# Optimization experiments

Measured on AMD Instinct MI355X. Metric: run time of the kernel, lower is better.

The kernel has to match this reference:

```python
import jax, jax.numpy as jnp
import numpy as np

B, T, F, H = 256, 512, 64, 512


def setup_inputs() -> dict:
    key = jax.random.key(0)
    ks = jax.random.split(key, 7)
    s_ih = 1.0 / np.sqrt(H)
    return {
        "x": jax.random.normal(ks[0], (B, T, F), dtype=jnp.float32),
        # PyTorch nn.GRU layout: rows ordered [reset; update; new], each (H, in)
        "W_ih": jax.random.uniform(ks[1], (3 * H, F), minval=-s_ih, maxval=s_ih, dtype=jnp.float32),
        "W_hh": jax.random.uniform(ks[2], (3 * H, H), minval=-s_ih, maxval=s_ih, dtype=jnp.float32),
        "b_ih": jax.random.uniform(ks[3], (3 * H,), minval=-s_ih, maxval=s_ih, dtype=jnp.float32),
        "b_hh": jax.random.uniform(ks[4], (3 * H,), minval=-s_ih, maxval=s_ih, dtype=jnp.float32),
        "head_w": jax.random.uniform(ks[5], (1, H), minval=-s_ih, maxval=s_ih, dtype=jnp.float32),
        "head_b": jax.random.uniform(ks[6], (1,), minval=-s_ih, maxval=s_ih, dtype=jnp.float32),
    }


def _gru_last_hidden(x, W_ih, W_hh, b_ih, b_hh):
    # Precompute input projections for all timesteps: (B, T, 3H)
    gi_all = jnp.einsum("btf,gf->btg", x, W_ih) + b_ih
    gi_all = jnp.swapaxes(gi_all, 0, 1)  # (T, B, 3H) for scan

    def step(h, gi):
        gh = h @ W_hh.T + b_hh  # (B, 3H)
        i_r, i_z, i_n = jnp.split(gi, 3, axis=-1)
        h_r, h_z, h_n = jnp.split(gh, 3, axis=-1)
        r = jax.nn.sigmoid(i_r + h_r)
        z = jax.nn.sigmoid(i_z + h_z)
        n = jnp.tanh(i_n + r * h_n)
        h_new = (1.0 - z) * n + z * h
        return h_new, None

    h0 = jnp.zeros((x.shape[0], W_hh.shape[1]), dtype=x.dtype)
    h_last, _ = jax.lax.scan(step, h0, gi_all)
    return h_last  # (B, H)


def reference(x, W_ih, W_hh, b_ih, b_hh, head_w, head_b):
    last = _gru_last_hidden(x, W_ih, W_hh, b_ih, b_hh)  # out[:, -1, :]
    # head_dropout is identity in eval mode
    y = last @ head_w.T + head_b  # (B, 1)
    return y.squeeze(-1)  # (B,)
```

## Files before the change

### kernel.cpp

```cpp
#include <hip/hip_runtime.h>
#include <hip/hip_bf16.h>

typedef __attribute__((ext_vector_type(4))) float f32x4;
typedef __attribute__((ext_vector_type(8))) short s16x8;
typedef __attribute__((ext_vector_type(4))) unsigned short u16x4;
typedef unsigned long long u64;
typedef unsigned int u32;

#define DEVFN static __device__ __forceinline__

constexpr int B_ = 256, T_ = 512, F_ = 64, H_ = 512;
constexpr int NB = 16;
constexpr int NS = 8;
constexpr int MT = B_ / NB;
constexpr int NT = H_ / NS;
constexpr int NGRID = NB * NS;
constexpr int NTHR = 256;
constexpr int C2 = H_ / 2;

DEVFN unsigned short f2bf(float f) {
  u32 u = __builtin_bit_cast(u32, f);
  u += 0x7fffu + ((u >> 16) & 1u);
  return (unsigned short)(u >> 16);
}

DEVFN float sigmoidf_(float x) { return 1.f / (1.f + __expf(-x)); }
DEVFN float tanhf_(float x) {
  float a = fabsf(x);
  float t = __expf(-2.f * a);
  float r = (1.f - t) / (1.f + t);
  return x < 0.f ? -r : r;
}

__global__ __launch_bounds__(NTHR, 1)
void gru_scan(const float* __restrict__ x, const float* __restrict__ Wih,
              const float* __restrict__ Whh, const float* __restrict__ bih,
              const float* __restrict__ bhh, const float* __restrict__ hw,
              const float* __restrict__ hb, float* __restrict__ out,
              u64* __restrict__ Hpk)
{
  const int tid = threadIdx.x;
  const int lane = tid & 63;
  const int wv = tid >> 6;
  const int gi = (int)blockIdx.x & (NB - 1);
  const int sj = (int)blockIdx.x >> 4;

  __shared__ __align__(16) unsigned char h_lds[2][MT * 1024];
  __shared__ __align__(16) unsigned char x_lds[2][MT * 128];

  const int frow = lane & 15;
  const int g8 = (lane >> 4) * 8;
  const int g16 = (lane >> 4) * 16;
  const int gc = sj * NT + wv * 16 + frow;

  s16x8 whh_f[3][16];
  s16x8 wih_f[3][2];
#pragma unroll
  for (int g = 0; g < 3; ++g) {
    const float* wr = Whh + ((size_t)(g * H_ + gc)) * H_;
#pragma unroll
    for (int kk = 0; kk < 16; ++kk) {
      const float4 p0 = *(const float4*)(wr + kk * 32 + g8);
      const float4 p1 = *(const float4*)(wr + kk * 32 + g8 + 4);
      s16x8 f;
      f[0] = (short)f2bf(p0.x); f[1] = (short)f2bf(p0.y);
      f[2] = (short)f2bf(p0.z); f[3] = (short)f2bf(p0.w);
      f[4] = (short)f2bf(p1.x); f[5] = (short)f2bf(p1.y);
      f[6] = (short)f2bf(p1.z); f[7] = (short)f2bf(p1.w);
      whh_f[g][kk] = f;
    }
    const float* wr2 = Wih + ((size_t)(g * H_ + gc)) * F_;
#pragma unroll
    for (int k2 = 0; k2 < 2; ++k2) {
      const float4 p0 = *(const float4*)(wr2 + k2 * 32 + g8);
      const float4 p1 = *(const float4*)(wr2 + k2 * 32 + g8 + 4);
      s16x8 f;
      f[0] = (short)f2bf(p0.x); f[1] = (short)f2bf(p0.y);
      f[2] = (short)f2bf(p0.z); f[3] = (short)f2bf(p0.w);
      f[4] = (short)f2bf(p1.x); f[5] = (short)f2bf(p1.y);
      f[6] = (short)f2bf(p1.z); f[7] = (short)f2bf(p1.w);
      wih_f[g][k2] = f;
    }
  }

  const float b_r  = bih[gc] + bhh[gc];
  const float b_z  = bih[H_ + gc] + bhh[H_ + gc];
  const float b_in = bih[2 * H_ + gc];
  const float b_hn = bhh[2 * H_ + gc];
  const float hw_l = hw[gc];

  const int aswz = (frow & 7) << 4;
  const int c2own = sj * 32 + wv * 8 + (frow >> 1);

  float hstate[4] = {0.f, 0.f, 0.f, 0.f};

  for (int t = 0; t < T_; ++t) {
    const int p = t & 1;
    if (t > 0) {
      const u64* src = Hpk + ((size_t)p * B_ + gi * MT) * C2 + tid;
      u64 pk[16];
#pragma unroll
      for (int q = 0; q < 16; ++q)
        pk[q] = __hip_atomic_load(src + q * C2, __ATOMIC_RELAXED,
                                  __HIP_MEMORY_SCOPE_AGENT);
      for (;;) {
        bool bad = false;
#pragma unroll
        for (int q = 0; q < 16; ++q) bad |= ((u32)(pk[q] >> 32) != (u32)t);
        if (!__any(bad)) break;
        __builtin_amdgcn_s_sleep(1);
#pragma unroll
        for (int q = 0; q < 16; ++q)
          if ((u32)(pk[q] >> 32) != (u32)t)
            pk[q] = __hip_atomic_load(src + q * C2, __ATOMIC_RELAXED,
                                      __HIP_MEMORY_SCOPE_AGENT);
      }
#pragma unroll
      for (int q = 0; q < 16; ++q)
        *(u32*)(&h_lds[p][q * 1024 + ((tid * 4) ^ ((q & 7) << 4))]) =
            (u32)pk[q];
    }
    {
      const int m = tid >> 4, fs = tid & 15;
      const float4 xv =
          *(const float4*)(x + (((size_t)(gi * MT + m)) * T_ + t) * F_ + fs * 4);
      u16x4 xb;
      xb[0] = f2bf(xv.x); xb[1] = f2bf(xv.y);
      xb[2] = f2bf(xv.z); xb[3] = f2bf(xv.w);
      *(u16x4*)(&x_lds[p][m * 128 + ((fs * 8) ^ ((m & 7) << 4))]) = xb;
    }
    __syncthreads();

    const char* xrow_ptr = (const char*)&x_lds[p][frow * 128];
    const char* hrow_ptr = (const char*)&h_lds[p][frow * 1024];
    f32x4 ar = {0.f, 0.f, 0.f, 0.f}, az = {0.f, 0.f, 0.f, 0.f};
    f32x4 anx = {0.f, 0.f, 0.f, 0.f}, anh = {0.f, 0.f, 0.f, 0.f};
#pragma unroll
    for (int k2 = 0; k2 < 2; ++k2) {
      const s16x8 a = *(const s16x8*)(xrow_ptr + ((k2 * 64 + g16) ^ aswz));
      ar  = __builtin_amdgcn_mfma_f32_16x16x32_bf16(a, wih_f[0][k2], ar, 0, 0, 0);
      az  = __builtin_amdgcn_mfma_f32_16x16x32_bf16(a, wih_f[1][k2], az, 0, 0, 0);
      anx = __builtin_amdgcn_mfma_f32_16x16x32_bf16(a, wih_f[2][k2], anx, 0, 0, 0);
    }
    if (t > 0) {
#pragma unroll
      for (int kk = 0; kk < 16; ++kk) {
        const s16x8 a = *(const s16x8*)(hrow_ptr + ((kk * 64 + g16) ^ aswz));
        ar  = __builtin_amdgcn_mfma_f32_16x16x32_bf16(a, whh_f[0][kk], ar, 0, 0, 0);
        az  = __builtin_amdgcn_mfma_f32_16x16x32_bf16(a, whh_f[1][kk], az, 0, 0, 0);
        anh = __builtin_amdgcn_mfma_f32_16x16x32_bf16(a, whh_f[2][kk], anh, 0, 0, 0);
      }
    }

#pragma unroll
    for (int e = 0; e < 4; ++e) {
      const float rr = sigmoidf_(ar[e] + b_r);
      const float zz = sigmoidf_(az[e] + b_z);
      const float nn = tanhf_(anx[e] + b_in + rr * (anh[e] + b_hn));
      hstate[e] = (1.f - zz) * nn + zz * hstate[e];
    }

    if (t < T_ - 1) {
      unsigned short hbf[4];
#pragma unroll
      for (int e = 0; e < 4; ++e) hbf[e] = f2bf(hstate[e]);
      u64* dstbase = Hpk + ((size_t)((t + 1) & 1) * B_ + gi * MT) * C2;
#pragma unroll
      for (int e = 0; e < 4; ++e) {
        const u32 other = (u32)__shfl_xor((int)hbf[e], 1);
        if (!(lane & 1)) {
          const int m = ((lane >> 4) << 2) + e;
          const u64 val = ((u64)(u32)(t + 1) << 32) |
                          (u64)((u32)hbf[e] | (other << 16));
          __hip_atomic_store(dstbase + m * C2 + c2own, val, __ATOMIC_RELAXED,
                             __HIP_MEMORY_SCOPE_AGENT);
        }
      }
    }
  }

  {
    float part[4];
#pragma unroll
    for (int e = 0; e < 4; ++e) part[e] = hstate[e] * hw_l;
#pragma unroll
    for (int mask = 1; mask < 16; mask <<= 1) {
#pragma unroll
      for (int e = 0; e < 4; ++e) part[e] += __shfl_xor(part[e], mask);
    }
    if ((lane & 15) == 0) {
      const float addb = (sj == 0 && wv == 0) ? hb[0] : 0.f;
#pragma unroll
      for (int e = 0; e < 4; ++e)
        atomicAdd(out + gi * MT + ((lane >> 4) << 2) + e, part[e] + addb);
    }
  }
}

extern "C" void kernel_launch(void* const* d_in, const int* in_sizes, int n_in,
                              void* d_out, int out_size, void* d_ws, size_t ws_size,
                              hipStream_t stream)
{
  const float* x   = (const float*)d_in[0];
  const float* Wih = (const float*)d_in[1];
  const float* Whh = (const float*)d_in[2];
  const float* bih = (const float*)d_in[3];
  const float* bhh = (const float*)d_in[4];
  const float* hw  = (const float*)d_in[5];
  const float* hb  = (const float*)d_in[6];
  float* out = (float*)d_out;
  u64* Hpk = (u64*)d_ws;

  hipMemsetAsync(d_out, 0, (size_t)out_size * sizeof(float), stream);

  gru_scan<<<dim3(NGRID), dim3(NTHR), 0, stream>>>(
      x, Wih, Whh, bih, bhh, hw, hb, out, Hpk);
}
```

Before: 1.933 ms.

## Poll hidden-state exchange with sc0 vector loads, falling back to atomic buffer

Each step's hidden-state packets are now written twice: once with a plain store to a fast buffer and once with an agent-scope atomic store to a slow buffer. Consumers poll the fast buffer with inline-asm global loads using the sc0 cache bit, which are cheaper than per-element atomic loads. After a spin limit they permanently switch to the atomic buffer so progress is still guaranteed. The x load is also hoisted before the wait so its latency overlaps the polling. The cost is doubled store traffic, and the fast path relies on visibility behaviour that plain stores and sc0 loads may not guarantee across compute units.

```diff
diff --git a/kernel.cpp b/kernel.cpp
--- a/kernel.cpp
+++ b/kernel.cpp
@@ -17,6 +17,7 @@
 constexpr int NGRID = NB * NS;
 constexpr int NTHR = 256;
 constexpr int C2 = H_ / 2;
+constexpr int SPIN_LIMIT = 2048;
 
 DEVFN unsigned short f2bf(float f) {
   u32 u = __builtin_bit_cast(u32, f);
@@ -37,7 +38,7 @@
               const float* __restrict__ Whh, const float* __restrict__ bih,
               const float* __restrict__ bhh, const float* __restrict__ hw,
               const float* __restrict__ hb, float* __restrict__ out,
-              u64* __restrict__ Hpk)
+              u64* __restrict__ HpkF, u64* __restrict__ HpkS)
 {
   const int tid = threadIdx.x;
   const int lane = tid & 63;
@@ -93,27 +94,63 @@
   const int c2own = sj * 32 + wv * 8 + (frow >> 1);
 
   float hstate[4] = {0.f, 0.f, 0.f, 0.f};
+  bool slow_mode = false;
 
   for (int t = 0; t < T_; ++t) {
     const int p = t & 1;
+    const int xm = tid >> 4, xfs = tid & 15;
+    const float4 xv =
+        *(const float4*)(x + (((size_t)(gi * MT + xm)) * T_ + t) * F_ + xfs * 4);
+
     if (t > 0) {
-      const u64* src = Hpk + ((size_t)p * B_ + gi * MT) * C2 + tid;
+      const size_t off = ((size_t)p * B_ + gi * MT) * C2 + tid;
+      const u64* fsrc = HpkF + off;
+      const u64* ssrc = HpkS + off;
       u64 pk[16];
-#pragma unroll
-      for (int q = 0; q < 16; ++q)
-        pk[q] = __hip_atomic_load(src + q * C2, __ATOMIC_RELAXED,
-                                  __HIP_MEMORY_SCOPE_AGENT);
+      if (!slow_mode) {
+#pragma unroll
+        for (int i = 0; i < 8; ++i) {
+          asm volatile(
+              "global_load_dwordx2 %0, %2, off sc0\n\t"
+              "global_load_dwordx2 %1, %2, off offset:2048 sc0"
+              : "=&v"(pk[2 * i]), "=&v"(pk[2 * i + 1])
+              : "v"(fsrc + i * 2 * C2)
+              : "memory");
+        }
+        asm volatile("s_waitcnt vmcnt(0)" ::: "memory");
+        __builtin_amdgcn_sched_barrier(0);
+      } else {
+#pragma unroll
+        for (int q = 0; q < 16; ++q)
+          pk[q] = __hip_atomic_load(ssrc + q * C2, __ATOMIC_RELAXED,
+                                    __HIP_MEMORY_SCOPE_AGENT);
+      }
+      int spins = 0;
       for (;;) {
         bool bad = false;
 #pragma unroll
         for (int q = 0; q < 16; ++q) bad |= ((u32)(pk[q] >> 32) != (u32)t);
         if (!__any(bad)) break;
+        if (++spins == SPIN_LIMIT) slow_mode = true;
         __builtin_amdgcn_s_sleep(1);
-#pragma unroll
-        for (int q = 0; q < 16; ++q)
-          if ((u32)(pk[q] >> 32) != (u32)t)
-            pk[q] = __hip_atomic_load(src + q * C2, __ATOMIC_RELAXED,
+        if (!slow_mode) {
+#pragma unroll
+          for (int i = 0; i < 8; ++i) {
+            asm volatile(
+                "global_load_dwordx2 %0, %2, off sc0\n\t"
+                "global_load_dwordx2 %1, %2, off offset:2048 sc0"
+                : "=&v"(pk[2 * i]), "=&v"(pk[2 * i + 1])
+                : "v"(fsrc + i * 2 * C2)
+                : "memory");
+          }
+          asm volatile("s_waitcnt vmcnt(0)" ::: "memory");
+          __builtin_amdgcn_sched_barrier(0);
+        } else {
+#pragma unroll
+          for (int q = 0; q < 16; ++q)
+            pk[q] = __hip_atomic_load(ssrc + q * C2, __ATOMIC_RELAXED,
                                       __HIP_MEMORY_SCOPE_AGENT);
+        }
       }
 #pragma unroll
       for (int q = 0; q < 16; ++q)
@@ -121,13 +158,10 @@
             (u32)pk[q];
     }
     {
-      const int m = tid >> 4, fs = tid & 15;
-      const float4 xv =
-          *(const float4*)(x + (((size_t)(gi * MT + m)) * T_ + t) * F_ + fs * 4);
       u16x4 xb;
       xb[0] = f2bf(xv.x); xb[1] = f2bf(xv.y);
       xb[2] = f2bf(xv.z); xb[3] = f2bf(xv.w);
-      *(u16x4*)(&x_lds[p][m * 128 + ((fs * 8) ^ ((m & 7) << 4))]) = xb;
+      *(u16x4*)(&x_lds[p][xm * 128 + ((xfs * 8) ^ ((xm & 7) << 4))]) = xb;
     }
     __syncthreads();
 
@@ -164,7 +198,7 @@
       unsigned short hbf[4];
 #pragma unroll
       for (int e = 0; e < 4; ++e) hbf[e] = f2bf(hstate[e]);
-      u64* dstbase = Hpk + ((size_t)((t + 1) & 1) * B_ + gi * MT) * C2;
+      const size_t pbase = ((size_t)((t + 1) & 1) * B_ + gi * MT) * C2;
 #pragma unroll
       for (int e = 0; e < 4; ++e) {
         const u32 other = (u32)__shfl_xor((int)hbf[e], 1);
@@ -172,7 +206,9 @@
           const int m = ((lane >> 4) << 2) + e;
           const u64 val = ((u64)(u32)(t + 1) << 32) |
                           (u64)((u32)hbf[e] | (other << 16));
-          __hip_atomic_store(dstbase + m * C2 + c2own, val, __ATOMIC_RELAXED,
+          const size_t idx = pbase + (size_t)m * C2 + c2own;
+          HpkF[idx] = val;
+          __hip_atomic_store(HpkS + idx, val, __ATOMIC_RELAXED,
                              __HIP_MEMORY_SCOPE_AGENT);
         }
       }
@@ -209,10 +245,11 @@
   const float* hw  = (const float*)d_in[5];
   const float* hb  = (const float*)d_in[6];
   float* out = (float*)d_out;
-  u64* Hpk = (u64*)d_ws;
+  u64* HpkF = (u64*)d_ws;
+  u64* HpkS = (u64*)((char*)d_ws + (1u << 20));
 
   hipMemsetAsync(d_out, 0, (size_t)out_size * sizeof(float), stream);
 
   gru_scan<<<dim3(NGRID), dim3(NTHR), 0, stream>>>(
-      x, Wih, Whh, bih, bhh, hw, hb, out, Hpk);
-}
+      x, Wih, Whh, bih, bhh, hw, hb, out, HpkF, HpkS);
+}
```

After: 5.656 ms. 2.93x slower.
